# Optimization experiments

Hardware: AMD Instinct MI355X
Metric: run time of the kernel (lower is better)

## Reference

```python
import jax, jax.numpy as jnp
import numpy as np

B, D, N, K, H = 32, 1024, 65536, 4096, 8

def setup_inputs() -> dict:
    key = jax.random.key(0)
    ks = jax.random.split(key, 8)
    s = D ** -0.5  # keep projections well-scaled
    return {
        "query": jax.random.normal(ks[0], (B, D), jnp.float32),
        "buffer": jax.random.normal(ks[1], (N, D), jnp.float32),
        "priorities": jax.random.normal(ks[2], (N,), jnp.float32),
        "Wq": jax.random.normal(ks[3], (D, D), jnp.float32) * s,
        "bq": jnp.zeros((D,), jnp.float32),
        "Wk": jax.random.normal(ks[4], (D, D), jnp.float32) * s,
        "bk": jnp.zeros((D,), jnp.float32),
        "Wv": jax.random.normal(ks[5], (D, D), jnp.float32) * s,
        "bv": jnp.zeros((D,), jnp.float32),
        "Wo": jax.random.normal(ks[6], (D, D), jnp.float32) * s,
        "bo": jnp.zeros((D,), jnp.float32),
        "top_k": K,
    }

def reference(query, buffer, priorities, Wq, bq, Wk, bk, Wv, bv, Wo, bo, top_k):
    # priority-based top-k selection (no_grad in original)
    _, idx = jax.lax.top_k(jax.lax.stop_gradient(priorities), top_k)
    subset = buffer[idx]                              # [K, D] gather; shared across batch
    hd = D // H
    scale = hd ** -0.5
    q = (query @ Wq + bq).reshape(B, H, hd)           # single-query attention (seq len 1)
    k = (subset @ Wk + bk).reshape(top_k, H, hd)
    v = (subset @ Wv + bv).reshape(top_k, H, hd)
    scores = jnp.einsum('bhd,khd->bhk', q, k) * scale  # [B, H, K]
    attn = jax.nn.softmax(scores, axis=-1)
    ctx = jnp.einsum('bhk,khd->bhd', attn, v).reshape(B, D)
    retrieved = ctx @ Wo + bo                          # [B, D]
    attn_avg = attn.mean(axis=1)                       # head-averaged weights [B, K]
    return retrieved, attn_avg
```

## Files before the change

kernel.cpp:

```cpp
#include <hip/hip_runtime.h>
#include <stdint.h>

typedef unsigned int u32;
typedef unsigned long long u64;
typedef uint16_t u16;

typedef short bf16x8 __attribute__((ext_vector_type(8)));
typedef float f32x4 __attribute__((ext_vector_type(4)));


__device__ __forceinline__ float bf2f(u16 x) { return __uint_as_float(((u32)x) << 16); }
__device__ __forceinline__ u16 f2bf(float f) {
    u32 u = __float_as_uint(f);
    return (u16)((u + 0x7FFF + ((u >> 16) & 1)) >> 16);
}


__global__ __launch_bounds__(256) void init_kernel(const float* __restrict__ prio,
                                                   u64* __restrict__ keys,
                                                   u32* __restrict__ hist,
                                                   u64* __restrict__ cand,
                                                   u32* __restrict__ scctl) {
    int i = blockIdx.x * 256 + threadIdx.x;
    u32 fb = __float_as_uint(prio[i]);
    u32 s = (fb & 0x80000000u) ? ~fb : (fb | 0x80000000u);
    keys[i] = ((u64)(~s) << 32) | (u64)i;
    hist[i] = 0;
    if (i < 8192) cand[i] = ~0ull;
    if (i < 4) scctl[i] = 0;
}

__global__ __launch_bounds__(256) void hist_kernel(const u64* __restrict__ keys,
                                                   u32* __restrict__ hist) {
    int i = blockIdx.x * 256 + threadIdx.x;
    atomicAdd(&hist[(u32)(keys[i] >> 48)], 1u);
}

__global__ __launch_bounds__(1024) void scan_kernel(const u32* __restrict__ hist,
                                                    u32* __restrict__ scctl) {
    int t = threadIdx.x;
    int base = t * 64;
    u32 s = 0;
    for (int i = 0; i < 64; ++i) s += hist[base + i];
    u32 inc = s;
    for (int o = 1; o < 64; o <<= 1) {
        u32 v = __shfl_up(inc, o);
        if ((t & 63) >= o) inc += v;
    }
    __shared__ u32 ws[16];
    if ((t & 63) == 63) ws[t >> 6] = inc;
    __syncthreads();
    if (t == 0) {
        u32 a = 0;
        for (int wv = 0; wv < 16; ++wv) { u32 x = ws[wv]; ws[wv] = a; a += x; }
    }
    __syncthreads();
    u32 incl = inc + ws[t >> 6];
    u32 excl = incl - s;
    if (excl < 4096u && incl >= 4096u) {
        u32 cum = excl;
        for (int i = 0; i < 64; ++i) {
            u32 c = hist[base + i];
            if (cum + c >= 4096u) { scctl[0] = (u32)(base + i); scctl[1] = cum; break; }
            cum += c;
        }
    }
}

__global__ __launch_bounds__(256) void compact_kernel(const u64* __restrict__ keys,
                                                      u64* __restrict__ cand,
                                                      u32* __restrict__ scctl) {
    int i = blockIdx.x * 256 + threadIdx.x;
    u64 k = keys[i];
    u32 bin = (u32)(k >> 48);
    u32 Tb = scctl[0];
    if (bin < Tb) {
        u32 p = atomicAdd(&scctl[2], 1u);
        cand[p] = k;
    } else if (bin == Tb) {
        u32 p = atomicAdd(&scctl[3], 1u);
        if (p < 4096u) cand[4096 + p] = k;
    }
}

__global__ __launch_bounds__(1024) void sort4096_kernel(u64* __restrict__ cand) {
    __shared__ u64 sh[4096];
    u64* src = cand + (size_t)blockIdx.x * 4096;
    int t = threadIdx.x;
    for (int i = t; i < 4096; i += 1024) sh[i] = src[i];
    __syncthreads();
    for (int k = 2; k <= 4096; k <<= 1) {
        for (int j = k >> 1; j >= 1; j >>= 1) {
            for (int v = t; v < 2048; v += 1024) {
                int i1 = ((v & ~(j - 1)) << 1) | (v & (j - 1));
                int i2 = i1 | j;
                bool up = ((i1 & k) == 0);
                u64 a = sh[i1], b = sh[i2];
                if ((a > b) == up) { sh[i1] = b; sh[i2] = a; }
            }
            __syncthreads();
        }
    }
    for (int i = t; i < 4096; i += 1024) src[i] = sh[i];
}

__global__ __launch_bounds__(256) void gather_convert_kernel(const float* __restrict__ buffer,
                                                             const u64* __restrict__ cand,
                                                             const u32* __restrict__ scctl,
                                                             u16* __restrict__ bsub) {
    int row = blockIdx.x;
    u32 S = scctl[1];
    u64 key = ((u32)row < S) ? cand[row] : cand[4096 + row - (int)S];
    u32 src_row = (u32)key;
    int c4 = threadIdx.x * 4;
    float4 v = *(const float4*)(buffer + (size_t)src_row * 1024 + c4);
    ushort4 r;
    r.x = f2bf(v.x); r.y = f2bf(v.y); r.z = f2bf(v.z); r.w = f2bf(v.w);
    *(ushort4*)(bsub + (size_t)row * 1024 + c4) = r;
}

__global__ __launch_bounds__(256) void transpose_bsub_kernel(const u16* __restrict__ bsub,
                                                             u16* __restrict__ bsubT) {
    int tx = blockIdx.x, ty = blockIdx.y, t = threadIdx.x;
    __shared__ u16 tile[64][65];
    for (int s = t; s < 4096; s += 256) {
        int r = s >> 6, c = s & 63;
        tile[r][c] = bsub[(size_t)(ty * 64 + r) * 1024 + tx * 64 + c];
    }
    __syncthreads();
    for (int s = t; s < 4096; s += 256) {
        int r = s >> 6, c = s & 63;
        bsubT[(size_t)(tx * 64 + r) * 4096 + ty * 64 + c] = tile[c][r];
    }
}

__global__ __launch_bounds__(256) void vecmat_kernel(const float* __restrict__ X,
                                                     const float* __restrict__ W,
                                                     const float* __restrict__ bias,
                                                     float* __restrict__ out) {
    int b = blockIdx.x, n0 = blockIdx.y * 64, t = threadIdx.x;
    __shared__ float xs[1024];
    __shared__ float red[4][64];
    for (int s = t; s < 1024; s += 256) xs[s] = X[b * 1024 + s];
    __syncthreads();
    int n = t & 63, kq = t >> 6;
    const float* Wp = W + (size_t)(kq * 256) * 1024 + n0 + n;
    const float* xp = xs + kq * 256;
    float acc = 0.f;
#pragma unroll 8
    for (int k = 0; k < 256; ++k) acc += xp[k] * Wp[(size_t)k * 1024];
    red[kq][n] = acc;
    __syncthreads();
    if (t < 64) out[b * 1024 + n0 + t] = red[0][t] + red[1][t] + red[2][t] + red[3][t] + bias[n0 + t];
}

__global__ __launch_bounds__(256) void s1_kernel(const float* __restrict__ qp,
                                                 const float* __restrict__ Wk,
                                                 const float* __restrict__ bk,
                                                 u16* __restrict__ S1,
                                                 float* __restrict__ cb) {
    int h = blockIdx.x, e0 = blockIdx.y * 64, t = threadIdx.x;
    __shared__ float qsh[32][128];
    __shared__ float wsh[64][132];
    for (int s = t; s < 4096; s += 256) {
        int b = s >> 7, d = s & 127;
        qsh[b][d] = qp[b * 1024 + h * 128 + d];
    }
    for (int s = t; s < 8192; s += 256) {
        int e = s >> 7, d = s & 127;
        wsh[e][d] = Wk[(size_t)(e0 + e) * 1024 + h * 128 + d];
    }
    __syncthreads();
    if (blockIdx.y == 0 && t < 32) {
        float a = 0.f;
        for (int d = 0; d < 128; ++d) a += qsh[t][d] * bk[h * 128 + d];
        cb[t * 8 + h] = a;
    }
    int e = t & 63, b0 = (t >> 6) * 8;
    float acc[8] = {0.f, 0.f, 0.f, 0.f, 0.f, 0.f, 0.f, 0.f};
#pragma unroll 4
    for (int d = 0; d < 128; d += 4) {
        float4 w = *(const float4*)&wsh[e][d];
#pragma unroll
        for (int bb = 0; bb < 8; ++bb) {
            float4 q = *(const float4*)&qsh[b0 + bb][d];
            acc[bb] += w.x * q.x + w.y * q.y + w.z * q.z + w.w * q.w;
        }
    }
#pragma unroll
    for (int bb = 0; bb < 8; ++bb)
        S1[(size_t)((b0 + bb) * 8 + h) * 1024 + e0 + e] = f2bf(acc[bb]);
}

__global__ __launch_bounds__(256) void gemm_scores_kernel(const u16* __restrict__ A,
                                                          const u16* __restrict__ B,
                                                          const float* __restrict__ cb,
                                                          float* __restrict__ out) {
    const int nt = blockIdx.x, mt = blockIdx.y;
    __shared__ __align__(16) u16 As[128 * 64];
    __shared__ __align__(16) u16 Bs[128 * 64];
    const int t = threadIdx.x, lane = t & 63, w = t >> 6;
    const int wm = (w >> 1) * 64, wn = (w & 1) * 64;
    const int q16 = lane >> 4, l15 = lane & 15;
    f32x4 acc[4][4];
#pragma unroll
    for (int i = 0; i < 4; i++)
#pragma unroll
        for (int j = 0; j < 4; j++) acc[i][j] = (f32x4){0.f, 0.f, 0.f, 0.f};
    const int sr = t >> 3, sc = t & 7;
    for (int kk = 0; kk < 1024; kk += 64) {
#pragma unroll
        for (int p = 0; p < 4; ++p) {
            int r = p * 32 + sr, pc = sc ^ (r & 7);
            uint4 va = *(const uint4*)(A + (size_t)(mt * 128 + r) * 1024 + kk + sc * 8);
            uint4 vb = *(const uint4*)(B + (size_t)(nt * 128 + r) * 1024 + kk + sc * 8);
            *(uint4*)&As[r * 64 + pc * 8] = va;
            *(uint4*)&Bs[r * 64 + pc * 8] = vb;
        }
        __syncthreads();
#pragma unroll
        for (int f = 0; f < 2; ++f) {
            bf16x8 a[4], b[4];
#pragma unroll
            for (int i = 0; i < 4; ++i) {
                int m = wm + i * 16 + l15;
                int pc = (f * 4 + q16) ^ (m & 7);
                a[i] = *(const bf16x8*)&As[m * 64 + pc * 8];
                int n = wn + i * 16 + l15;
                b[i] = *(const bf16x8*)&Bs[n * 64 + pc * 8];
            }
#pragma unroll
            for (int i = 0; i < 4; ++i)
#pragma unroll
                for (int j = 0; j < 4; ++j)
                    acc[i][j] = __builtin_amdgcn_mfma_f32_16x16x32_bf16(a[i], b[j], acc[i][j], 0, 0, 0);
        }
        __syncthreads();
    }
#pragma unroll
    for (int i = 0; i < 4; ++i) {
        int mbase = mt * 128 + wm + i * 16 + q16 * 4;
        float cbv[4];
#pragma unroll
        for (int r = 0; r < 4; ++r) cbv[r] = cb[mbase + r];
#pragma unroll
        for (int j = 0; j < 4; ++j) {
            int n = nt * 128 + wn + j * 16 + l15;
#pragma unroll
            for (int r = 0; r < 4; ++r)
                out[(size_t)(mbase + r) * 4096 + n] = acc[i][j][r] * 0.08838834764831845f + cbv[r];
        }
    }
}

__global__ __launch_bounds__(256) void softmax_kernel(const float* __restrict__ scores,
                                                      u16* __restrict__ attnbf) {
    int row = blockIdx.x, t = threadIdx.x;
    __shared__ float rowsh[4096];
    __shared__ float red[4];
    const float* p = scores + (size_t)row * 4096;
    float m = -1e30f;
    for (int i = t; i < 4096; i += 256) {
        float v = p[i];
        rowsh[i] = v;
        m = fmaxf(m, v);
    }
#pragma unroll
    for (int o = 32; o >= 1; o >>= 1) m = fmaxf(m, __shfl_xor(m, o));
    if ((t & 63) == 0) red[t >> 6] = m;
    __syncthreads();
    m = fmaxf(fmaxf(red[0], red[1]), fmaxf(red[2], red[3]));
    float sum = 0.f;
    for (int i = t; i < 4096; i += 256) {
        float e = __expf(rowsh[i] - m);
        rowsh[i] = e;
        sum += e;
    }
#pragma unroll
    for (int o = 32; o >= 1; o >>= 1) sum += __shfl_xor(sum, o);
    __syncthreads();
    if ((t & 63) == 0) red[t >> 6] = sum;
    __syncthreads();
    sum = red[0] + red[1] + red[2] + red[3];
    float inv = 1.0f / sum;
    for (int i = t; i < 4096; i += 256)
        attnbf[(size_t)row * 4096 + i] = f2bf(rowsh[i] * inv);
}

__global__ __launch_bounds__(256) void attn_avg_kernel(const u16* __restrict__ attnbf,
                                                       float* __restrict__ out) {
    int g = blockIdx.x * 256 + threadIdx.x;
    int b = g >> 12, k = g & 4095;
    float s = 0.f;
#pragma unroll
    for (int h = 0; h < 8; ++h) s += bf2f(attnbf[(size_t)(b * 8 + h) * 4096 + k]);
    out[g] = s * 0.125f;
}

__global__ __launch_bounds__(256) void gemm_t_kernel(const u16* __restrict__ A,
                                                     const u16* __restrict__ B,
                                                     float* __restrict__ part) {
    const int nt = blockIdx.x, mt = blockIdx.y, ks = blockIdx.z;
    __shared__ __align__(16) u16 As[128 * 64];
    __shared__ __align__(16) u16 Bs[128 * 64];
    const int t = threadIdx.x, lane = t & 63, w = t >> 6;
    const int wm = (w >> 1) * 64, wn = (w & 1) * 64;
    const int q16 = lane >> 4, l15 = lane & 15;
    f32x4 acc[4][4];
#pragma unroll
    for (int i = 0; i < 4; i++)
#pragma unroll
        for (int j = 0; j < 4; j++) acc[i][j] = (f32x4){0.f, 0.f, 0.f, 0.f};
    const int sr = t >> 3, sc = t & 7;
    const int k0 = ks * 512;
    for (int kk = k0; kk < k0 + 512; kk += 64) {
#pragma unroll
        for (int p = 0; p < 4; ++p) {
            int r = p * 32 + sr, pc = sc ^ (r & 7);
            uint4 va = *(const uint4*)(A + (size_t)(mt * 128 + r) * 4096 + kk + sc * 8);
            uint4 vb = *(const uint4*)(B + (size_t)(nt * 128 + r) * 4096 + kk + sc * 8);
            *(uint4*)&As[r * 64 + pc * 8] = va;
            *(uint4*)&Bs[r * 64 + pc * 8] = vb;
        }
        __syncthreads();
#pragma unroll
        for (int f = 0; f < 2; ++f) {
            bf16x8 a[4], b[4];
#pragma unroll
            for (int i = 0; i < 4; ++i) {
                int m = wm + i * 16 + l15;
                int pc = (f * 4 + q16) ^ (m & 7);
                a[i] = *(const bf16x8*)&As[m * 64 + pc * 8];
                int n = wn + i * 16 + l15;
                b[i] = *(const bf16x8*)&Bs[n * 64 + pc * 8];
            }
#pragma unroll
            for (int i = 0; i < 4; ++i)
#pragma unroll
                for (int j = 0; j < 4; ++j)
                    acc[i][j] = __builtin_amdgcn_mfma_f32_16x16x32_bf16(a[i], b[j], acc[i][j], 0, 0, 0);
        }
        __syncthreads();
    }
#pragma unroll
    for (int i = 0; i < 4; ++i) {
        int mbase = mt * 128 + wm + i * 16 + q16 * 4;
#pragma unroll
        for (int j = 0; j < 4; ++j) {
            int n = nt * 128 + wn + j * 16 + l15;
#pragma unroll
            for (int r = 0; r < 4; ++r)
                part[(size_t)(ks * 256 + mbase + r) * 1024 + n] = acc[i][j][r];
        }
    }
}

__global__ __launch_bounds__(256) void ctx_reduce_kernel(const float* __restrict__ part,
                                                         const float* __restrict__ Wv,
                                                         const float* __restrict__ bv,
                                                         float* __restrict__ ctx) {
    int b = blockIdx.x, n0 = blockIdx.y * 64, t = threadIdx.x;
    int h = n0 >> 7;
    int bh = b * 8 + h;
    __shared__ float ts[1024];
    __shared__ float red[4][64];
    for (int s = t; s < 1024; s += 256) {
        float a = 0.f;
#pragma unroll
        for (int ks = 0; ks < 8; ++ks) a += part[(size_t)(ks * 256 + bh) * 1024 + s];
        ts[s] = a;
    }
    __syncthreads();
    int n = t & 63, kq = t >> 6;
    const float* Wp = Wv + (size_t)(kq * 256) * 1024 + n0 + n;
    const float* tp = ts + kq * 256;
    float acc = 0.f;
#pragma unroll 8
    for (int k = 0; k < 256; ++k) acc += tp[k] * Wp[(size_t)k * 1024];
    red[kq][n] = acc;
    __syncthreads();
    if (t < 64) ctx[b * 1024 + n0 + t] = red[0][t] + red[1][t] + red[2][t] + red[3][t] + bv[n0 + t];
}

extern "C" void kernel_launch(void* const* d_in, const int* in_sizes, int n_in,
                              void* d_out, int out_size, void* d_ws, size_t ws_size,
                              hipStream_t stream) {
    const float* query  = (const float*)d_in[0];
    const float* buffer = (const float*)d_in[1];
    const float* prio   = (const float*)d_in[2];
    const float* Wq     = (const float*)d_in[3];
    const float* bq     = (const float*)d_in[4];
    const float* Wk     = (const float*)d_in[5];
    const float* bk     = (const float*)d_in[6];
    const float* Wv     = (const float*)d_in[7];
    const float* bv     = (const float*)d_in[8];
    const float* Wo     = (const float*)d_in[9];
    const float* bo     = (const float*)d_in[10];

    char* w = (char*)d_ws;
    auto alloc = [&](size_t bytes) {
        char* p = w;
        w += (bytes + 255) & ~(size_t)255;
        return p;
    };
    u64* keys    = (u64*)alloc((size_t)65536 * 8);
    u32* hist    = (u32*)alloc((size_t)65536 * 4);
    u32* scctl   = (u32*)alloc(16);
    u64* cand    = (u64*)alloc((size_t)8192 * 8);
    u16* bsub    = (u16*)alloc((size_t)4096 * 1024 * 2);
    u16* bsubT   = (u16*)alloc((size_t)1024 * 4096 * 2);
    float* qp    = (float*)alloc((size_t)32 * 1024 * 4);
    u16* S1bf    = (u16*)alloc((size_t)256 * 1024 * 2);
    float* cbb   = (float*)alloc((size_t)256 * 4);
    float* scores= (float*)alloc((size_t)256 * 4096 * 4);
    u16* attnbf  = (u16*)alloc((size_t)256 * 4096 * 2);
    float* Tpart = (float*)alloc((size_t)8 * 256 * 1024 * 4);
    float* ctx   = (float*)alloc((size_t)32 * 1024 * 4);

    float* out_retrieved = (float*)d_out;
    float* out_attnavg   = (float*)d_out + 32768;

    init_kernel<<<256, 256, 0, stream>>>(prio, keys, hist, cand, scctl);
    hist_kernel<<<256, 256, 0, stream>>>(keys, hist);
    scan_kernel<<<1, 1024, 0, stream>>>(hist, scctl);
    compact_kernel<<<256, 256, 0, stream>>>(keys, cand, scctl);
    sort4096_kernel<<<2, 1024, 0, stream>>>(cand);

    gather_convert_kernel<<<4096, 256, 0, stream>>>(buffer, cand, scctl, bsub);
    transpose_bsub_kernel<<<dim3(16, 64), 256, 0, stream>>>(bsub, bsubT);
    vecmat_kernel<<<dim3(32, 16), 256, 0, stream>>>(query, Wq, bq, qp);

    s1_kernel<<<dim3(8, 16), 256, 0, stream>>>(qp, Wk, bk, S1bf, cbb);
    gemm_scores_kernel<<<dim3(32, 2), 256, 0, stream>>>(S1bf, bsub, cbb, scores);

    softmax_kernel<<<256, 256, 0, stream>>>(scores, attnbf);
    attn_avg_kernel<<<512, 256, 0, stream>>>(attnbf, out_attnavg);

    gemm_t_kernel<<<dim3(8, 2, 8), 256, 0, stream>>>(attnbf, bsubT, Tpart);
    ctx_reduce_kernel<<<dim3(32, 16), 256, 0, stream>>>(Tpart, Wv, bv, ctx);

    vecmat_kernel<<<dim3(32, 16), 256, 0, stream>>>(ctx, Wo, bo, out_retrieved);
}
```

Baseline: 540.3 us.

## Fuse gather with transpose, register bitonic sort, batch vecmat over four rows

Merges the gather+bf16 convert and the transpose into one kernel that writes both bsub and bsubT from a shared tile, removing one full pass over the 4096x1024 subset. The bitonic sort keeps four elements per thread in registers and uses wave shuffles for small strides, touching shared memory only for large strides. vecmat and ctx_reduce now process four batch rows per block, so each weight load is reused four times. The scan vectorizes its histogram reads. These cut memory traffic and syncs, but the fused gather uses only 128 blocks, which may leave the GPU under-occupied.

Result: slower. 557.3 us (+3.2%).

```diff
diff --git a/kernel.cpp b/kernel.cpp
--- a/kernel.cpp
+++ b/kernel.cpp
@@ -40,8 +40,13 @@
                                                     u32* __restrict__ scctl) {
     int t = threadIdx.x;
     int base = t * 64;
+    const uint4* hp = (const uint4*)(hist + base);
     u32 s = 0;
-    for (int i = 0; i < 64; ++i) s += hist[base + i];
+#pragma unroll
+    for (int i = 0; i < 16; ++i) {
+        uint4 h4 = hp[i];
+        s += h4.x + h4.y + h4.z + h4.w;
+    }
     u32 inc = s;
     for (int o = 1; o < 64; o <<= 1) {
         u32 v = __shfl_up(inc, o);
@@ -87,71 +92,122 @@
     __shared__ u64 sh[4096];
     u64* src = cand + (size_t)blockIdx.x * 4096;
     int t = threadIdx.x;
-    for (int i = t; i < 4096; i += 1024) sh[i] = src[i];
-    __syncthreads();
+    u64 v[4];
+#pragma unroll
+    for (int s = 0; s < 4; ++s) v[s] = src[t * 4 + s];
     for (int k = 2; k <= 4096; k <<= 1) {
         for (int j = k >> 1; j >= 1; j >>= 1) {
-            for (int v = t; v < 2048; v += 1024) {
-                int i1 = ((v & ~(j - 1)) << 1) | (v & (j - 1));
-                int i2 = i1 | j;
-                bool up = ((i1 & k) == 0);
-                u64 a = sh[i1], b = sh[i2];
-                if ((a > b) == up) { sh[i1] = b; sh[i2] = a; }
+            if (j >= 256) {
+                __syncthreads();
+#pragma unroll
+                for (int s = 0; s < 4; ++s) sh[t * 4 + s] = v[s];
+                __syncthreads();
+#pragma unroll
+                for (int s = 0; s < 4; ++s) {
+                    int i = t * 4 + s;
+                    u64 p = sh[i ^ j];
+                    bool keepmin = (((i & k) == 0) == ((i & j) == 0));
+                    v[s] = keepmin ? (v[s] < p ? v[s] : p) : (v[s] > p ? v[s] : p);
+                }
+            } else if (j >= 4) {
+                int ld = j >> 2;
+#pragma unroll
+                for (int s = 0; s < 4; ++s) {
+                    int i = t * 4 + s;
+                    u64 p = __shfl_xor(v[s], ld, 64);
+                    bool keepmin = (((i & k) == 0) == ((i & j) == 0));
+                    v[s] = keepmin ? (v[s] < p ? v[s] : p) : (v[s] > p ? v[s] : p);
+                }
+            } else if (j == 2) {
+#pragma unroll
+                for (int s = 0; s < 2; ++s) {
+                    int i = t * 4 + s;
+                    bool up = ((i & k) == 0);
+                    u64 a = v[s], b = v[s + 2];
+                    if ((a > b) == up) { v[s] = b; v[s + 2] = a; }
+                }
+            } else {
+#pragma unroll
+                for (int s = 0; s < 4; s += 2) {
+                    int i = t * 4 + s;
+                    bool up = ((i & k) == 0);
+                    u64 a = v[s], b = v[s + 1];
+                    if ((a > b) == up) { v[s] = b; v[s + 1] = a; }
+                }
             }
-            __syncthreads();
-        }
-    }
-    for (int i = t; i < 4096; i += 1024) src[i] = sh[i];
-}
-
-__global__ __launch_bounds__(256) void gather_convert_kernel(const float* __restrict__ buffer,
-                                                             const u64* __restrict__ cand,
-                                                             const u32* __restrict__ scctl,
-                                                             u16* __restrict__ bsub) {
-    int row = blockIdx.x;
-    u32 S = scctl[1];
-    u64 key = ((u32)row < S) ? cand[row] : cand[4096 + row - (int)S];
-    u32 src_row = (u32)key;
-    int c4 = threadIdx.x * 4;
-    float4 v = *(const float4*)(buffer + (size_t)src_row * 1024 + c4);
-    ushort4 r;
-    r.x = f2bf(v.x); r.y = f2bf(v.y); r.z = f2bf(v.z); r.w = f2bf(v.w);
-    *(ushort4*)(bsub + (size_t)row * 1024 + c4) = r;
-}
-
-__global__ __launch_bounds__(256) void transpose_bsub_kernel(const u16* __restrict__ bsub,
-                                                             u16* __restrict__ bsubT) {
-    int tx = blockIdx.x, ty = blockIdx.y, t = threadIdx.x;
-    __shared__ u16 tile[64][65];
+        }
+    }
+#pragma unroll
+    for (int s = 0; s < 4; ++s) src[t * 4 + s] = v[s];
+}
+
+__global__ __launch_bounds__(256) void gather_transpose_kernel(const float* __restrict__ buffer,
+                                                               const u64* __restrict__ cand,
+                                                               const u32* __restrict__ scctl,
+                                                               u16* __restrict__ bsub,
+                                                               u16* __restrict__ bsubT) {
+    int r0 = blockIdx.x * 32;
+    int t = threadIdx.x;
+    __shared__ u16 tile[32][65];
+    __shared__ u32 rowidx[32];
+    if (t < 32) {
+        int row = r0 + t;
+        u32 S = scctl[1];
+        u64 key = ((u32)row < S) ? cand[row] : cand[4096 + row - (int)S];
+        rowidx[t] = (u32)key;
+    }
+    __syncthreads();
+    for (int c0 = 0; c0 < 1024; c0 += 64) {
+        for (int s = t; s < 512; s += 256) {
+            int r = s >> 4, c4 = (s & 15) * 4;
+            float4 vv = *(const float4*)(buffer + (size_t)rowidx[r] * 1024 + c0 + c4);
+            ushort4 o;
+            o.x = f2bf(vv.x); o.y = f2bf(vv.y); o.z = f2bf(vv.z); o.w = f2bf(vv.w);
+            *(ushort4*)(bsub + (size_t)(r0 + r) * 1024 + c0 + c4) = o;
+            tile[r][c4] = o.x; tile[r][c4 + 1] = o.y; tile[r][c4 + 2] = o.z; tile[r][c4 + 3] = o.w;
+        }
+        __syncthreads();
+        for (int s = t; s < 1024; s += 256) {
+            int rT = s >> 4;
+            int cT = (s & 15) * 2;
+            ushort2 o2;
+            o2.x = tile[cT][rT];
+            o2.y = tile[cT + 1][rT];
+            *(ushort2*)(bsubT + (size_t)(c0 + rT) * 4096 + r0 + cT) = o2;
+        }
+        __syncthreads();
+    }
+}
+
+__global__ __launch_bounds__(256) void vecmat4_kernel(const float* __restrict__ X,
+                                                      const float* __restrict__ W,
+                                                      const float* __restrict__ bias,
+                                                      float* __restrict__ out) {
+    int bg = blockIdx.x, n0 = blockIdx.y * 64, t = threadIdx.x;
+    __shared__ float xs[4][1024];
+    __shared__ float red[4][4][64];
     for (int s = t; s < 4096; s += 256) {
-        int r = s >> 6, c = s & 63;
-        tile[r][c] = bsub[(size_t)(ty * 64 + r) * 1024 + tx * 64 + c];
-    }
-    __syncthreads();
-    for (int s = t; s < 4096; s += 256) {
-        int r = s >> 6, c = s & 63;
-        bsubT[(size_t)(tx * 64 + r) * 4096 + ty * 64 + c] = tile[c][r];
-    }
-}
-
-__global__ __launch_bounds__(256) void vecmat_kernel(const float* __restrict__ X,
-                                                     const float* __restrict__ W,
-                                                     const float* __restrict__ bias,
-                                                     float* __restrict__ out) {
-    int b = blockIdx.x, n0 = blockIdx.y * 64, t = threadIdx.x;
-    __shared__ float xs[1024];
-    __shared__ float red[4][64];
-    for (int s = t; s < 1024; s += 256) xs[s] = X[b * 1024 + s];
+        int bb = s >> 10, k = s & 1023;
+        xs[bb][k] = X[(bg * 4 + bb) * 1024 + k];
+    }
     __syncthreads();
     int n = t & 63, kq = t >> 6;
     const float* Wp = W + (size_t)(kq * 256) * 1024 + n0 + n;
-    const float* xp = xs + kq * 256;
-    float acc = 0.f;
+    const float* x0 = xs[0] + kq * 256;
+    const float* x1 = xs[1] + kq * 256;
+    const float* x2 = xs[2] + kq * 256;
+    const float* x3 = xs[3] + kq * 256;
+    float a0 = 0.f, a1 = 0.f, a2 = 0.f, a3 = 0.f;
 #pragma unroll 8
-    for (int k = 0; k < 256; ++k) acc += xp[k] * Wp[(size_t)k * 1024];
-    red[kq][n] = acc;
-    __syncthreads();
-    if (t < 64) out[b * 1024 + n0 + t] = red[0][t] + red[1][t] + red[2][t] + red[3][t] + bias[n0 + t];
+    for (int k = 0; k < 256; ++k) {
+        float w = Wp[(size_t)k * 1024];
+        a0 += x0[k] * w; a1 += x1[k] * w; a2 += x2[k] * w; a3 += x3[k] * w;
+    }
+    red[kq][0][n] = a0; red[kq][1][n] = a1; red[kq][2][n] = a2; red[kq][3][n] = a3;
+    __syncthreads();
+    int bb = t >> 6;
+    out[(bg * 4 + bb) * 1024 + n0 + n] =
+        red[0][bb][n] + red[1][bb][n] + red[2][bb][n] + red[3][bb][n] + bias[n0 + n];
 }
 
 __global__ __launch_bounds__(256) void s1_kernel(const float* __restrict__ qp,
@@ -287,8 +343,8 @@
         attnbf[(size_t)row * 4096 + i] = f2bf(rowsh[i] * inv);
 }
 
-__global__ __launch_bounds__(256) void attn_avg_kernel(const u16* __restrict__ attnbf,
-                                                       float* __restrict__ out) {
+__global__ void attn_avg_kernel(const u16* __restrict__ attnbf,
+                                float* __restrict__ out) {
     int g = blockIdx.x * 256 + threadIdx.x;
     int b = g >> 12, k = g & 4095;
     float s = 0.f;
@@ -355,31 +411,40 @@
     }
 }
 
-__global__ __launch_bounds__(256) void ctx_reduce_kernel(const float* __restrict__ part,
-                                                         const float* __restrict__ Wv,
-                                                         const float* __restrict__ bv,
-                                                         float* __restrict__ ctx) {
-    int b = blockIdx.x, n0 = blockIdx.y * 64, t = threadIdx.x;
+__global__ __launch_bounds__(256) void ctx_reduce4_kernel(const float* __restrict__ part,
+                                                          const float* __restrict__ Wv,
+                                                          const float* __restrict__ bv,
+                                                          float* __restrict__ ctx) {
+    int bg = blockIdx.x, n0 = blockIdx.y * 64, t = threadIdx.x;
     int h = n0 >> 7;
-    int bh = b * 8 + h;
-    __shared__ float ts[1024];
-    __shared__ float red[4][64];
-    for (int s = t; s < 1024; s += 256) {
+    __shared__ float ts[4][1024];
+    __shared__ float red[4][4][64];
+    for (int s = t; s < 4096; s += 256) {
+        int bb = s >> 10, e = s & 1023;
+        int bh = (bg * 4 + bb) * 8 + h;
         float a = 0.f;
 #pragma unroll
-        for (int ks = 0; ks < 8; ++ks) a += part[(size_t)(ks * 256 + bh) * 1024 + s];
-        ts[s] = a;
+        for (int ks = 0; ks < 8; ++ks) a += part[(size_t)(ks * 256 + bh) * 1024 + e];
+        ts[bb][e] = a;
     }
     __syncthreads();
     int n = t & 63, kq = t >> 6;
     const float* Wp = Wv + (size_t)(kq * 256) * 1024 + n0 + n;
-    const float* tp = ts + kq * 256;
-    float acc = 0.f;
+    const float* x0 = ts[0] + kq * 256;
+    const float* x1 = ts[1] + kq * 256;
+    const float* x2 = ts[2] + kq * 256;
+    const float* x3 = ts[3] + kq * 256;
+    float a0 = 0.f, a1 = 0.f, a2 = 0.f, a3 = 0.f;
 #pragma unroll 8
-    for (int k = 0; k < 256; ++k) acc += tp[k] * Wp[(size_t)k * 1024];
-    red[kq][n] = acc;
-    __syncthreads();
-    if (t < 64) ctx[b * 1024 + n0 + t] = red[0][t] + red[1][t] + red[2][t] + red[3][t] + bv[n0 + t];
+    for (int k = 0; k < 256; ++k) {
+        float w = Wp[(size_t)k * 1024];
+        a0 += x0[k] * w; a1 += x1[k] * w; a2 += x2[k] * w; a3 += x3[k] * w;
+    }
+    red[kq][0][n] = a0; red[kq][1][n] = a1; red[kq][2][n] = a2; red[kq][3][n] = a3;
+    __syncthreads();
+    int bb = t >> 6;
+    ctx[(bg * 4 + bb) * 1024 + n0 + n] =
+        red[0][bb][n] + red[1][bb][n] + red[2][bb][n] + red[3][bb][n] + bv[n0 + n];
 }
 
 extern "C" void kernel_launch(void* const* d_in, const int* in_sizes, int n_in,
@@ -426,9 +491,8 @@
     compact_kernel<<<256, 256, 0, stream>>>(keys, cand, scctl);
     sort4096_kernel<<<2, 1024, 0, stream>>>(cand);
 
-    gather_convert_kernel<<<4096, 256, 0, stream>>>(buffer, cand, scctl, bsub);
-    transpose_bsub_kernel<<<dim3(16, 64), 256, 0, stream>>>(bsub, bsubT);
-    vecmat_kernel<<<dim3(32, 16), 256, 0, stream>>>(query, Wq, bq, qp);
+    gather_transpose_kernel<<<128, 256, 0, stream>>>(buffer, cand, scctl, bsub, bsubT);
+    vecmat4_kernel<<<dim3(8, 16), 256, 0, stream>>>(query, Wq, bq, qp);
 
     s1_kernel<<<dim3(8, 16), 256, 0, stream>>>(qp, Wk, bk, S1bf, cbb);
     gemm_scores_kernel<<<dim3(32, 2), 256, 0, stream>>>(S1bf, bsub, cbb, scores);
@@ -437,7 +501,7 @@
     attn_avg_kernel<<<512, 256, 0, stream>>>(attnbf, out_attnavg);
 
     gemm_t_kernel<<<dim3(8, 2, 8), 256, 0, stream>>>(attnbf, bsubT, Tpart);
-    ctx_reduce_kernel<<<dim3(32, 16), 256, 0, stream>>>(Tpart, Wv, bv, ctx);
-
-    vecmat_kernel<<<dim3(32, 16), 256, 0, stream>>>(ctx, Wo, bo, out_retrieved);
-}
+    ctx_reduce4_kernel<<<dim3(8, 16), 256, 0, stream>>>(Tpart, Wv, bv, ctx);
+
+    vecmat4_kernel<<<dim3(8, 16), 256, 0, stream>>>(ctx, Wo, bo, out_retrieved);
+}
```
